# Performance work log

Measured on AMD Instinct MI355X. Metric: run time of the kernel, lower is better.

Reference implementation:

```python
import jax, jax.numpy as jnp
import numpy as np

B, L, D, H = 1, 2048, 1024, 16
DH = D // H            # head dim = 64
RD = 16                # rope dim = dim_head / 4 (partial RoPE)
SCALE = DH ** -0.5
NEG = -1e9


def _layernorm(x, g, b, eps=1e-5):
    m = jnp.mean(x, -1, keepdims=True)
    v = jnp.mean((x - m) ** 2, -1, keepdims=True)
    return (x - m) * jax.lax.rsqrt(v + eps) * g + b


def _rope_tables(length, rd):
    # GPT-NeoX style: freqs over rd/2, duplicated via concat
    inv_freq = 1.0 / (10000.0 ** (jnp.arange(0, rd, 2, dtype=jnp.float32) / rd))
    t = jnp.arange(length, dtype=jnp.float32)
    f = t[:, None] * inv_freq[None, :]          # [L, rd/2]
    f = jnp.concatenate([f, f], -1)             # [L, rd]
    return jnp.cos(f)[None, None], jnp.sin(f)[None, None]  # [1,1,L,rd]


def _apply_rope(x, cos, sin):
    # rotate only the first RD dims of each head; pass the rest through
    rd = cos.shape[-1]
    xr, xp = x[..., :rd], x[..., rd:]
    x1, x2 = jnp.split(xr, 2, axis=-1)
    rot = jnp.concatenate([-x2, x1], -1)
    return jnp.concatenate([xr * cos + rot * sin, xp], -1)


def _alibi_causal_bias(length, num_heads):
    # per-head ALiBi slope + causal mask (AttentionBiasMask: ['alibi','causal'])
    slopes = 2.0 ** (-8.0 * (jnp.arange(num_heads, dtype=jnp.float32) + 1) / num_heads)
    i = jnp.arange(length)
    rel = i[:, None] - i[None, :]               # [L, L], >=0 on/below diagonal
    bias = -slopes[:, None, None] * rel[None].astype(jnp.float32)
    bias = jnp.where(rel[None] >= 0, bias, NEG)  # causal mask
    return bias[None]                            # [1, H, L, L]


def setup_inputs() -> dict:
    key = jax.random.key(0)
    ks = jax.random.split(key, 8)
    s = 0.02
    return {
        "x": jax.random.normal(ks[0], (B, L, D), jnp.float32),
        "previous_attn_dots": jax.random.normal(ks[1], (B, H, L, L), jnp.float32) * 0.1,
        "Wq": jax.random.normal(ks[2], (D, D), jnp.float32) * s,
        "Wk": jax.random.normal(ks[3], (D, D), jnp.float32) * s,
        "Wv": jax.random.normal(ks[4], (D, D), jnp.float32) * s,
        "Wo": jax.random.normal(ks[5], (D, D), jnp.float32) * s,
        "bo": jnp.zeros((D,), jnp.float32),
        "gamma": jnp.ones((D,), jnp.float32),
        "beta": jnp.zeros((D,), jnp.float32),
        "Wg": jax.random.normal(ks[6], (D, D), jnp.float32) * s,
        "bg": jnp.zeros((D,), jnp.float32),
    }


def reference(x, previous_attn_dots, Wq, Wk, Wv, Wo, bo, gamma, beta, Wg, bg):
    residual = x
    cos, sin = _rope_tables(L, RD)
    bias = _alibi_causal_bias(L, H)

    h = _layernorm(x, gamma, beta)

    def heads(t):  # [B,L,D] -> [B,H,L,DH]
        return t.reshape(B, L, H, DH).transpose(0, 2, 1, 3)

    q = _apply_rope(heads(h @ Wq), cos, sin)
    k = _apply_rope(heads(h @ Wk), cos, sin)
    v = _apply_rope(heads(h @ Wv), cos, sin)  # rotate_v_bool=True

    dots = jnp.einsum('bhid,bhjd->bhij', q, k) * SCALE
    dots = dots + previous_attn_dots          # residual attention
    dots = dots + bias                        # ALiBi + causal
    attn_map = jax.nn.softmax(dots, axis=-1)

    o = jnp.einsum('bhij,bhjd->bhid', attn_map, v)
    o = o.transpose(0, 2, 1, 3).reshape(B, L, D)
    y = o @ Wo + bo

    gate = jax.nn.sigmoid(residual @ Wg + bg)  # output_gate ('sigmoid','on_residual')
    y = gate * y
    y = y + residual                           # add_residual
    return (y, attn_map, dots)
```

## Files before the change

### kernel.cpp

```cpp
#include <hip/hip_runtime.h>
#include <hip/hip_bf16.h>
#include <math.h>

#define LLEN 2048
#define DMODEL 1024
#define NHEAD 16
#define DHEAD 64
#define SCALE 0.125f
#define NEGF -1000000000.0f

typedef __attribute__((ext_vector_type(8))) short short8;
typedef __attribute__((ext_vector_type(4))) float f32x4;

__device__ __forceinline__ unsigned short f2bf(float f) {
  union { float f; unsigned u; } cv; cv.f = f;
  unsigned u = cv.u;
  u += 0x7FFF + ((u >> 16) & 1);
  return (unsigned short)(u >> 16);
}

__global__ __launch_bounds__(256) void transpose_w(
    const float* __restrict__ Wq, const float* __restrict__ Wk,
    const float* __restrict__ Wv, const float* __restrict__ Wo,
    const float* __restrict__ Wg,
    unsigned short* __restrict__ Wqt, unsigned short* __restrict__ Wkt,
    unsigned short* __restrict__ Wvt, unsigned short* __restrict__ Wot,
    unsigned short* __restrict__ Wgt) {
  const float* W; unsigned short* Wt;
  switch (blockIdx.z) {
    case 0: W = Wq; Wt = Wqt; break;
    case 1: W = Wk; Wt = Wkt; break;
    case 2: W = Wv; Wt = Wvt; break;
    case 3: W = Wo; Wt = Wot; break;
    default: W = Wg; Wt = Wgt; break;
  }
  __shared__ unsigned short tile[64][72];
  int k0 = blockIdx.y * 64, n0 = blockIdx.x * 64;
  int c4 = (threadIdx.x & 15) * 4, r = threadIdx.x >> 4;
  for (int rr = r; rr < 64; rr += 16) {
    float4 v = *(const float4*)(W + (size_t)(k0 + rr) * DMODEL + n0 + c4);
    tile[rr][c4 + 0] = f2bf(v.x); tile[rr][c4 + 1] = f2bf(v.y);
    tile[rr][c4 + 2] = f2bf(v.z); tile[rr][c4 + 3] = f2bf(v.w);
  }
  __syncthreads();
  for (int rr = r; rr < 64; rr += 16) {
    ushort4 o;
    o.x = tile[c4 + 0][rr]; o.y = tile[c4 + 1][rr];
    o.z = tile[c4 + 2][rr]; o.w = tile[c4 + 3][rr];
    *(ushort4*)(Wt + (size_t)(n0 + rr) * DMODEL + k0 + c4) = o;
  }
}

__global__ __launch_bounds__(256) void ln_kernel(
    const float* __restrict__ x, const float* __restrict__ gamma,
    const float* __restrict__ beta,
    unsigned short* __restrict__ hb, unsigned short* __restrict__ xb) {
  int l = blockIdx.x, t = threadIdx.x;
  float4 v = ((const float4*)(x + (size_t)l * DMODEL))[t];
  float s  = v.x + v.y + v.z + v.w;
  float s2 = v.x * v.x + v.y * v.y + v.z * v.z + v.w * v.w;
  for (int off = 32; off; off >>= 1) {
    s  += __shfl_down(s, off);
    s2 += __shfl_down(s2, off);
  }
  __shared__ float rs[4], rs2[4];
  int wave = t >> 6, lane = t & 63;
  if (lane == 0) { rs[wave] = s; rs2[wave] = s2; }
  __syncthreads();
  float mean = (rs[0] + rs[1] + rs[2] + rs[3]) * (1.0f / DMODEL);
  float var  = (rs2[0] + rs2[1] + rs2[2] + rs2[3]) * (1.0f / DMODEL) - mean * mean;
  float rstd = rsqrtf(var + 1e-5f);
  float4 g = ((const float4*)gamma)[t];
  float4 b = ((const float4*)beta)[t];
  ushort4 hh, xx;
  hh.x = f2bf((v.x - mean) * rstd * g.x + b.x);
  hh.y = f2bf((v.y - mean) * rstd * g.y + b.y);
  hh.z = f2bf((v.z - mean) * rstd * g.z + b.z);
  hh.w = f2bf((v.w - mean) * rstd * g.w + b.w);
  xx.x = f2bf(v.x); xx.y = f2bf(v.y); xx.z = f2bf(v.z); xx.w = f2bf(v.w);
  ((ushort4*)(hb + (size_t)l * DMODEL))[t] = hh;
  ((ushort4*)(xb + (size_t)l * DMODEL))[t] = xx;
}

__device__ __forceinline__ void mfma_gemm_64x64(
    const unsigned short* __restrict__ A, const unsigned short* __restrict__ Bt,
    int row0, int ncol0, int lm, int quad, f32x4 acc[4]) {
  for (int k0 = 0; k0 < DMODEL; k0 += 64) {
    short8 a0 = *(const short8*)(A + (size_t)(row0 + lm) * DMODEL + k0 + quad * 8);
    short8 a1 = *(const short8*)(A + (size_t)(row0 + lm) * DMODEL + k0 + 32 + quad * 8);
#pragma unroll
    for (int c = 0; c < 4; c++) {
      const unsigned short* bp = Bt + (size_t)(ncol0 + c * 16 + lm) * DMODEL + k0 + quad * 8;
      short8 b0 = *(const short8*)(bp);
      short8 b1 = *(const short8*)(bp + 32);
      acc[c] = __builtin_amdgcn_mfma_f32_16x16x32_bf16(a0, b0, acc[c], 0, 0, 0);
      acc[c] = __builtin_amdgcn_mfma_f32_16x16x32_bf16(a1, b1, acc[c], 0, 0, 0);
    }
  }
}

__global__ __launch_bounds__(256) void gemm_qkv(
    const unsigned short* __restrict__ hb,
    const unsigned short* __restrict__ Wqt, const unsigned short* __restrict__ Wkt,
    const unsigned short* __restrict__ Wvt,
    unsigned short* __restrict__ qb, unsigned short* __restrict__ kb,
    unsigned short* __restrict__ vT) {
  int which = blockIdx.z;
  const unsigned short* Bt = (which == 0) ? Wqt : (which == 1) ? Wkt : Wvt;
  int wave = threadIdx.x >> 6, lane = threadIdx.x & 63;
  int lm = lane & 15, quad = lane >> 4;
  int it = blockIdx.x, head = blockIdx.y;
  int row0 = it * 64 + wave * 16;
  f32x4 acc[4] = {};
  mfma_gemm_64x64(hb, Bt, row0, head * 64, lm, quad, acc);
  __shared__ float tile[64][65];
#pragma unroll
  for (int c = 0; c < 4; c++)
#pragma unroll
    for (int r2 = 0; r2 < 4; r2++)
      tile[wave * 16 + quad * 4 + r2][c * 16 + lm] = acc[c][r2];
  __syncthreads();
  int r = threadIdx.x >> 2, seg = threadIdx.x & 3;
  int lrow = it * 64 + r;
  float vals[16];
#pragma unroll
  for (int i2 = 0; i2 < 16; i2++) vals[i2] = tile[r][seg * 16 + i2];
  if (seg == 0) {
    float outv[16];
#pragma unroll
    for (int j = 0; j < 8; j++) {
      float invf = powf(10000.f, -(float)j * 0.125f);
      float f = (float)lrow * invf;
      float cs = cosf(f), sn = sinf(f);
      outv[j]     = vals[j] * cs - vals[j + 8] * sn;
      outv[j + 8] = vals[j + 8] * cs + vals[j] * sn;
    }
#pragma unroll
    for (int j = 0; j < 16; j++) vals[j] = outv[j];
  }
  if (which < 2) {
    unsigned short* dst = ((which == 0) ? qb : kb) + ((size_t)head * LLEN + lrow) * DHEAD + seg * 16;
    union { unsigned short u[16]; uint4 v[2]; } tmp;
#pragma unroll
    for (int i2 = 0; i2 < 16; i2++) tmp.u[i2] = f2bf(vals[i2]);
    *(uint4*)dst = tmp.v[0];
    *((uint4*)dst + 1) = tmp.v[1];
  } else {
    __syncthreads();
#pragma unroll
    for (int i2 = 0; i2 < 16; i2++) tile[r][seg * 16 + i2] = vals[i2];
    __syncthreads();
    int dh = threadIdx.x >> 2, ls = threadIdx.x & 3;
    union { unsigned short u[16]; uint4 v[2]; } tmp;
#pragma unroll
    for (int i2 = 0; i2 < 16; i2++) tmp.u[i2] = f2bf(tile[ls * 16 + i2][dh]);
    unsigned short* dst = vT + ((size_t)head * DHEAD + dh) * LLEN + it * 64 + ls * 16;
    *(uint4*)dst = tmp.v[0];
    *((uint4*)dst + 1) = tmp.v[1];
  }
}

__global__ __launch_bounds__(128) void attn_kernel(
    const unsigned short* __restrict__ qb, const unsigned short* __restrict__ kb,
    const unsigned short* __restrict__ vT, const float* __restrict__ prev,
    float* __restrict__ dots, unsigned short* __restrict__ ob,
    float* __restrict__ rinvg) {
  int h = blockIdx.y;
  int wv = threadIdx.x >> 6, lane = threadIdx.x & 63;
  int lm = lane & 15, quad = lane >> 4;
  int g0 = blockIdx.x * 2 + wv;
  const unsigned short* q = qb + (size_t)h * LLEN * DHEAD;
  const unsigned short* k = kb + (size_t)h * LLEN * DHEAD;
  const unsigned short* v = vT + (size_t)h * DHEAD * LLEN;
  const float* pr = prev + (size_t)h * LLEN * LLEN;
  float* drow = dots + (size_t)h * LLEN * LLEN;
  float slope = exp2f(-8.0f * (float)(h + 1) / (float)NHEAD);
  __shared__ __align__(16) unsigned short pt[2][16][72];

  for (int pass = 0; pass < 2; ++pass) {
    int g = pass ? (127 - g0) : g0;
    int row0 = g * 16;
    int jt_end = g >> 2;
    short8 qa0 = *(const short8*)(q + (size_t)(row0 + lm) * DHEAD + quad * 8);
    short8 qa1 = *(const short8*)(q + (size_t)(row0 + lm) * DHEAD + 32 + quad * 8);
    f32x4 oacc[4] = {};
    float lsum[4] = {0.f, 0.f, 0.f, 0.f};
    for (int jt = 0; jt <= jt_end; jt++) {
      f32x4 s[4];
#pragma unroll
      for (int c = 0; c < 4; c++) {
        const unsigned short* kp = k + (size_t)(jt * 64 + c * 16 + lm) * DHEAD + quad * 8;
        short8 b0 = *(const short8*)kp;
        short8 b1 = *(const short8*)(kp + 32);
        f32x4 z = {};
        z = __builtin_amdgcn_mfma_f32_16x16x32_bf16(qa0, b0, z, 0, 0, 0);
        z = __builtin_amdgcn_mfma_f32_16x16x32_bf16(qa1, b1, z, 0, 0, 0);
        s[c] = z;
      }
#pragma unroll
      for (int c = 0; c < 4; c++) {
        int j = jt * 64 + c * 16 + lm;
#pragma unroll
        for (int r = 0; r < 4; r++) {
          int i = row0 + quad * 4 + r;
          int rel = i - j;
          float bias = (rel >= 0) ? (-slope * (float)rel) : NEGF;
          float d = fmaf(s[c][r], SCALE, pr[(size_t)i * LLEN + j]) + bias;
          drow[(size_t)i * LLEN + j] = d;
          float p = __expf(d);
          lsum[r] += p;
          pt[wv][quad * 4 + r][c * 16 + lm] = f2bf(p);
        }
      }
      short8 pa0 = *(const short8*)&pt[wv][lm][quad * 8];
      short8 pa1 = *(const short8*)&pt[wv][lm][32 + quad * 8];
#pragma unroll
      for (int c = 0; c < 4; c++) {
        const unsigned short* vp = v + (size_t)(c * 16 + lm) * LLEN + jt * 64 + quad * 8;
        short8 b0 = *(const short8*)vp;
        short8 b1 = *(const short8*)(vp + 32);
        oacc[c] = __builtin_amdgcn_mfma_f32_16x16x32_bf16(pa0, b0, oacc[c], 0, 0, 0);
        oacc[c] = __builtin_amdgcn_mfma_f32_16x16x32_bf16(pa1, b1, oacc[c], 0, 0, 0);
      }
    }
    float rv[4];
#pragma unroll
    for (int r = 0; r < 4; r++) {
      float sm = lsum[r];
#pragma unroll
      for (int off = 1; off < 16; off <<= 1) sm += __shfl_xor(sm, off, 16);
      rv[r] = 1.0f / sm;
    }
#pragma unroll
    for (int c = 0; c < 4; c++)
#pragma unroll
      for (int r = 0; r < 4; r++)
        ob[(size_t)(row0 + quad * 4 + r) * DMODEL + h * DHEAD + c * 16 + lm] =
            f2bf(oacc[c][r] * rv[r]);
    if (lm == 0) {
#pragma unroll
      for (int r = 0; r < 4; r++)
        rinvg[(size_t)h * LLEN + row0 + quad * 4 + r] = rv[r];
    }
    int jstart = (jt_end + 1) * 64;
    int ncols4 = (LLEN - jstart) >> 2;
    if (ncols4 > 0) {
      float4 negv = {NEGF, NEGF, NEGF, NEGF};
      int r = lane >> 2, t4 = lane & 3;
      size_t base = (size_t)(row0 + r) * LLEN + jstart;
      for (int c4 = t4; c4 < ncols4; c4 += 4)
        *(float4*)(drow + base + c4 * 4) = negv;
    }
  }
}

__global__ __launch_bounds__(256) void attn_norm(
    const float* __restrict__ dots, const float* __restrict__ rinvg,
    float* __restrict__ attn) {
  int h = blockIdx.y;
  int i0 = blockIdx.x * 8;
  const float* dr = dots + (size_t)h * LLEN * LLEN;
  float* ar = attn + (size_t)h * LLEN * LLEN;
#pragma unroll
  for (int rr = 0; rr < 8; rr++) {
    int i = i0 + rr;
    float rinv = rinvg[(size_t)h * LLEN + i];
    int nwr4 = ((i >> 6) + 1) * 16;
#pragma unroll
    for (int jc = 0; jc < 2; jc++) {
      int j4 = threadIdx.x + jc * 256;
      size_t idx = (size_t)i * LLEN + (size_t)j4 * 4;
      if (j4 < nwr4) {
        float4 d = *(const float4*)(dr + idx);
        float4 o;
        o.x = __expf(d.x) * rinv;
        o.y = __expf(d.y) * rinv;
        o.z = __expf(d.z) * rinv;
        o.w = __expf(d.w) * rinv;
        *(float4*)(ar + idx) = o;
      } else {
        float4 z = {0.f, 0.f, 0.f, 0.f};
        *(float4*)(ar + idx) = z;
      }
    }
  }
}

__global__ __launch_bounds__(256) void gemm_gate(
    const unsigned short* __restrict__ xb, const unsigned short* __restrict__ Wgt,
    const float* __restrict__ bg, float* __restrict__ gate) {
  int wave = threadIdx.x >> 6, lane = threadIdx.x & 63;
  int lm = lane & 15, quad = lane >> 4;
  int row0 = blockIdx.x * 64 + wave * 16, ncol0 = blockIdx.y * 64;
  f32x4 acc[4] = {};
  mfma_gemm_64x64(xb, Wgt, row0, ncol0, lm, quad, acc);
#pragma unroll
  for (int c = 0; c < 4; c++) {
    int col = ncol0 + c * 16 + lm;
    float bgv = bg[col];
#pragma unroll
    for (int r = 0; r < 4; r++) {
      int i = row0 + quad * 4 + r;
      float g = acc[c][r] + bgv;
      gate[(size_t)i * DMODEL + col] = 1.0f / (1.0f + __expf(-g));
    }
  }
}

__global__ __launch_bounds__(256) void gemm_out(
    const unsigned short* __restrict__ ob, const unsigned short* __restrict__ Wot,
    const float* __restrict__ bo, const float* __restrict__ gate,
    const float* __restrict__ x, float* __restrict__ y) {
  int wave = threadIdx.x >> 6, lane = threadIdx.x & 63;
  int lm = lane & 15, quad = lane >> 4;
  int row0 = blockIdx.x * 64 + wave * 16, ncol0 = blockIdx.y * 64;
  f32x4 acc[4] = {};
  mfma_gemm_64x64(ob, Wot, row0, ncol0, lm, quad, acc);
#pragma unroll
  for (int c = 0; c < 4; c++) {
    int col = ncol0 + c * 16 + lm;
    float bov = bo[col];
#pragma unroll
    for (int r = 0; r < 4; r++) {
      int i = row0 + quad * 4 + r;
      size_t idx = (size_t)i * DMODEL + col;
      float y0 = acc[c][r] + bov;
      y[idx] = gate[idx] * y0 + x[idx];
    }
  }
}

extern "C" void kernel_launch(void* const* d_in, const int* in_sizes, int n_in,
                              void* d_out, int out_size, void* d_ws, size_t ws_size,
                              hipStream_t stream) {
  const float* x     = (const float*)d_in[0];
  const float* prev  = (const float*)d_in[1];
  const float* Wq    = (const float*)d_in[2];
  const float* Wk    = (const float*)d_in[3];
  const float* Wv    = (const float*)d_in[4];
  const float* Wo    = (const float*)d_in[5];
  const float* bo    = (const float*)d_in[6];
  const float* gamma = (const float*)d_in[7];
  const float* beta  = (const float*)d_in[8];
  const float* Wg    = (const float*)d_in[9];
  const float* bg    = (const float*)d_in[10];

  float* y    = (float*)d_out;
  float* attn = y + 2097152;
  float* dots = attn + 67108864;

  char* ws = (char*)d_ws;
  unsigned short* hb  = (unsigned short*)(ws + 0);
  unsigned short* xb  = (unsigned short*)(ws + 4194304);
  unsigned short* Wqt = (unsigned short*)(ws + 8388608);
  unsigned short* Wkt = (unsigned short*)(ws + 10485760);
  unsigned short* Wvt = (unsigned short*)(ws + 12582912);
  unsigned short* Wot = (unsigned short*)(ws + 14680064);
  unsigned short* Wgt = (unsigned short*)(ws + 16777216);
  unsigned short* qb  = (unsigned short*)(ws + 18874368);
  unsigned short* kb  = (unsigned short*)(ws + 23068672);
  unsigned short* vT  = (unsigned short*)(ws + 27262976);
  unsigned short* ob  = (unsigned short*)(ws + 31457280);
  float*          gate = (float*)(ws + 35651584);
  float*          rinvg = (float*)(ws + 0);

  transpose_w<<<dim3(16, 16, 5), 256, 0, stream>>>(Wq, Wk, Wv, Wo, Wg, Wqt, Wkt, Wvt, Wot, Wgt);
  ln_kernel<<<dim3(2048), 256, 0, stream>>>(x, gamma, beta, hb, xb);
  gemm_qkv<<<dim3(32, 16, 3), 256, 0, stream>>>(hb, Wqt, Wkt, Wvt, qb, kb, vT);
  attn_kernel<<<dim3(32, 16), 128, 0, stream>>>(qb, kb, vT, prev, dots, ob, rinvg);
  attn_norm<<<dim3(256, 16), 256, 0, stream>>>(dots, rinvg, attn);
  gemm_gate<<<dim3(32, 16), 256, 0, stream>>>(xb, Wgt, bg, gate);
  gemm_out<<<dim3(32, 16), 256, 0, stream>>>(ob, Wot, bo, gate, x, y);
}
```

Baseline: 1.216 ms.

## Split attention KV tiles across four waves per row block and fuse gate/out GEMMs

The attention kernel now gives each 16-row query block (per head) its own 256-thread block. The four waves stride over KV tiles and combine partial outputs and row sums through shared memory, replacing the earlier two-wave blocks that each paired two row groups for load balance. This exposes far more parallelism (2048 blocks) for the memory-bound dots/prev traffic, at the cost of an LDS reduction and reduced per-wave work. Separately, the gate GEMM and output GEMM are fused into one kernel, which removes the intermediate gate buffer write and read and one launch.

```diff
diff --git a/kernel.cpp b/kernel.cpp
--- a/kernel.cpp
+++ b/kernel.cpp
@@ -160,97 +160,114 @@
   }
 }
 
-__global__ __launch_bounds__(128) void attn_kernel(
+__global__ __launch_bounds__(256, 4) void attn_kernel(
     const unsigned short* __restrict__ qb, const unsigned short* __restrict__ kb,
     const unsigned short* __restrict__ vT, const float* __restrict__ prev,
     float* __restrict__ dots, unsigned short* __restrict__ ob,
     float* __restrict__ rinvg) {
-  int h = blockIdx.y;
+  int bid = blockIdx.x;
+  int h = bid & 15, g = bid >> 4;
   int wv = threadIdx.x >> 6, lane = threadIdx.x & 63;
   int lm = lane & 15, quad = lane >> 4;
-  int g0 = blockIdx.x * 2 + wv;
+  int row0 = g * 16;
+  int jt_end = g >> 2;
   const unsigned short* q = qb + (size_t)h * LLEN * DHEAD;
   const unsigned short* k = kb + (size_t)h * LLEN * DHEAD;
   const unsigned short* v = vT + (size_t)h * DHEAD * LLEN;
   const float* pr = prev + (size_t)h * LLEN * LLEN;
   float* drow = dots + (size_t)h * LLEN * LLEN;
   float slope = exp2f(-8.0f * (float)(h + 1) / (float)NHEAD);
-  __shared__ __align__(16) unsigned short pt[2][16][72];
-
-  for (int pass = 0; pass < 2; ++pass) {
-    int g = pass ? (127 - g0) : g0;
-    int row0 = g * 16;
-    int jt_end = g >> 2;
-    short8 qa0 = *(const short8*)(q + (size_t)(row0 + lm) * DHEAD + quad * 8);
-    short8 qa1 = *(const short8*)(q + (size_t)(row0 + lm) * DHEAD + 32 + quad * 8);
-    f32x4 oacc[4] = {};
-    float lsum[4] = {0.f, 0.f, 0.f, 0.f};
-    for (int jt = 0; jt <= jt_end; jt++) {
-      f32x4 s[4];
-#pragma unroll
-      for (int c = 0; c < 4; c++) {
-        const unsigned short* kp = k + (size_t)(jt * 64 + c * 16 + lm) * DHEAD + quad * 8;
-        short8 b0 = *(const short8*)kp;
-        short8 b1 = *(const short8*)(kp + 32);
-        f32x4 z = {};
-        z = __builtin_amdgcn_mfma_f32_16x16x32_bf16(qa0, b0, z, 0, 0, 0);
-        z = __builtin_amdgcn_mfma_f32_16x16x32_bf16(qa1, b1, z, 0, 0, 0);
-        s[c] = z;
+
+  __shared__ __align__(16) char smem[16640];
+  unsigned short (*pt)[16][72] = (unsigned short (*)[16][72])smem;
+  float (*red)[64][16] = (float (*)[64][16])smem;
+  float* redl = (float*)(smem + 16384);
+
+  short8 qa0 = *(const short8*)(q + (size_t)(row0 + lm) * DHEAD + quad * 8);
+  short8 qa1 = *(const short8*)(q + (size_t)(row0 + lm) * DHEAD + 32 + quad * 8);
+  f32x4 oacc[4] = {};
+  float lsum[4] = {0.f, 0.f, 0.f, 0.f};
+
+  for (int jt = wv; jt <= jt_end; jt += 4) {
+    f32x4 s[4];
+#pragma unroll
+    for (int c = 0; c < 4; c++) {
+      const unsigned short* kp = k + (size_t)(jt * 64 + c * 16 + lm) * DHEAD + quad * 8;
+      short8 b0 = *(const short8*)kp;
+      short8 b1 = *(const short8*)(kp + 32);
+      f32x4 z = {};
+      z = __builtin_amdgcn_mfma_f32_16x16x32_bf16(qa0, b0, z, 0, 0, 0);
+      z = __builtin_amdgcn_mfma_f32_16x16x32_bf16(qa1, b1, z, 0, 0, 0);
+      s[c] = z;
+    }
+#pragma unroll
+    for (int c = 0; c < 4; c++) {
+      int j = jt * 64 + c * 16 + lm;
+#pragma unroll
+      for (int r = 0; r < 4; r++) {
+        int i = row0 + quad * 4 + r;
+        int rel = i - j;
+        float bias = (rel >= 0) ? (-slope * (float)rel) : NEGF;
+        float d = fmaf(s[c][r], SCALE, pr[(size_t)i * LLEN + j]) + bias;
+        drow[(size_t)i * LLEN + j] = d;
+        float p = __expf(d);
+        lsum[r] += p;
+        pt[wv][quad * 4 + r][c * 16 + lm] = f2bf(p);
       }
-#pragma unroll
-      for (int c = 0; c < 4; c++) {
-        int j = jt * 64 + c * 16 + lm;
-#pragma unroll
-        for (int r = 0; r < 4; r++) {
-          int i = row0 + quad * 4 + r;
-          int rel = i - j;
-          float bias = (rel >= 0) ? (-slope * (float)rel) : NEGF;
-          float d = fmaf(s[c][r], SCALE, pr[(size_t)i * LLEN + j]) + bias;
-          drow[(size_t)i * LLEN + j] = d;
-          float p = __expf(d);
-          lsum[r] += p;
-          pt[wv][quad * 4 + r][c * 16 + lm] = f2bf(p);
-        }
-      }
-      short8 pa0 = *(const short8*)&pt[wv][lm][quad * 8];
-      short8 pa1 = *(const short8*)&pt[wv][lm][32 + quad * 8];
-#pragma unroll
-      for (int c = 0; c < 4; c++) {
-        const unsigned short* vp = v + (size_t)(c * 16 + lm) * LLEN + jt * 64 + quad * 8;
-        short8 b0 = *(const short8*)vp;
-        short8 b1 = *(const short8*)(vp + 32);
-        oacc[c] = __builtin_amdgcn_mfma_f32_16x16x32_bf16(pa0, b0, oacc[c], 0, 0, 0);
-        oacc[c] = __builtin_amdgcn_mfma_f32_16x16x32_bf16(pa1, b1, oacc[c], 0, 0, 0);
-      }
-    }
-    float rv[4];
-#pragma unroll
-    for (int r = 0; r < 4; r++) {
-      float sm = lsum[r];
-#pragma unroll
-      for (int off = 1; off < 16; off <<= 1) sm += __shfl_xor(sm, off, 16);
-      rv[r] = 1.0f / sm;
-    }
-#pragma unroll
-    for (int c = 0; c < 4; c++)
-#pragma unroll
-      for (int r = 0; r < 4; r++)
-        ob[(size_t)(row0 + quad * 4 + r) * DMODEL + h * DHEAD + c * 16 + lm] =
-            f2bf(oacc[c][r] * rv[r]);
-    if (lm == 0) {
-#pragma unroll
-      for (int r = 0; r < 4; r++)
-        rinvg[(size_t)h * LLEN + row0 + quad * 4 + r] = rv[r];
-    }
-    int jstart = (jt_end + 1) * 64;
-    int ncols4 = (LLEN - jstart) >> 2;
-    if (ncols4 > 0) {
-      float4 negv = {NEGF, NEGF, NEGF, NEGF};
-      int r = lane >> 2, t4 = lane & 3;
-      size_t base = (size_t)(row0 + r) * LLEN + jstart;
-      for (int c4 = t4; c4 < ncols4; c4 += 4)
-        *(float4*)(drow + base + c4 * 4) = negv;
-    }
+    }
+    short8 pa0 = *(const short8*)&pt[wv][lm][quad * 8];
+    short8 pa1 = *(const short8*)&pt[wv][lm][32 + quad * 8];
+#pragma unroll
+    for (int c = 0; c < 4; c++) {
+      const unsigned short* vp = v + (size_t)(c * 16 + lm) * LLEN + jt * 64 + quad * 8;
+      short8 b0 = *(const short8*)vp;
+      short8 b1 = *(const short8*)(vp + 32);
+      oacc[c] = __builtin_amdgcn_mfma_f32_16x16x32_bf16(pa0, b0, oacc[c], 0, 0, 0);
+      oacc[c] = __builtin_amdgcn_mfma_f32_16x16x32_bf16(pa1, b1, oacc[c], 0, 0, 0);
+    }
+  }
+#pragma unroll
+  for (int r = 0; r < 4; r++) {
+#pragma unroll
+    for (int off = 1; off < 16; off <<= 1) lsum[r] += __shfl_xor(lsum[r], off, 16);
+  }
+  __syncthreads();
+#pragma unroll
+  for (int c = 0; c < 4; c++)
+#pragma unroll
+    for (int r = 0; r < 4; r++)
+      red[wv][lane][c * 4 + r] = oacc[c][r];
+  if (lm == 0) {
+#pragma unroll
+    for (int r = 0; r < 4; r++) redl[wv * 16 + quad * 4 + r] = lsum[r];
+  }
+  __syncthreads();
+  {
+    int t = threadIdx.x;
+    int ln = t & 63, idx0 = t >> 6;
+    int qd = ln >> 4, lmm = ln & 15;
+#pragma unroll
+    for (int kk = 0; kk < 4; kk++) {
+      int idx = idx0 * 4 + kk;
+      int c = idx >> 2, r = idx & 3;
+      float sv = red[0][ln][idx] + red[1][ln][idx] + red[2][ln][idx] + red[3][ln][idx];
+      int rr = qd * 4 + r;
+      float rs = redl[rr] + redl[16 + rr] + redl[32 + rr] + redl[48 + rr];
+      ob[(size_t)(row0 + rr) * DMODEL + h * DHEAD + c * 16 + lmm] = f2bf(sv / rs);
+    }
+    if (t < 16) {
+      float rs = redl[t] + redl[16 + t] + redl[32 + t] + redl[48 + t];
+      rinvg[(size_t)h * LLEN + row0 + t] = 1.0f / rs;
+    }
+  }
+  int jstart = (jt_end + 1) * 64;
+  int ncols4 = (LLEN - jstart) >> 2;
+  if (ncols4 > 0) {
+    float4 negv = {NEGF, NEGF, NEGF, NEGF};
+    int r = threadIdx.x >> 4, t16 = threadIdx.x & 15;
+    size_t base = (size_t)(row0 + r) * LLEN + jstart;
+    for (int c4 = t16; c4 < ncols4; c4 += 16)
+      *(float4*)(drow + base + c4 * 4) = negv;
   }
 }
 
@@ -286,46 +303,45 @@
   }
 }
 
-__global__ __launch_bounds__(256) void gemm_gate(
+__global__ __launch_bounds__(256) void gemm_gateout(
     const unsigned short* __restrict__ xb, const unsigned short* __restrict__ Wgt,
-    const float* __restrict__ bg, float* __restrict__ gate) {
-  int wave = threadIdx.x >> 6, lane = threadIdx.x & 63;
-  int lm = lane & 15, quad = lane >> 4;
-  int row0 = blockIdx.x * 64 + wave * 16, ncol0 = blockIdx.y * 64;
-  f32x4 acc[4] = {};
-  mfma_gemm_64x64(xb, Wgt, row0, ncol0, lm, quad, acc);
-#pragma unroll
-  for (int c = 0; c < 4; c++) {
-    int col = ncol0 + c * 16 + lm;
-    float bgv = bg[col];
-#pragma unroll
-    for (int r = 0; r < 4; r++) {
-      int i = row0 + quad * 4 + r;
-      float g = acc[c][r] + bgv;
-      gate[(size_t)i * DMODEL + col] = 1.0f / (1.0f + __expf(-g));
-    }
-  }
-}
-
-__global__ __launch_bounds__(256) void gemm_out(
+    const float* __restrict__ bg,
     const unsigned short* __restrict__ ob, const unsigned short* __restrict__ Wot,
-    const float* __restrict__ bo, const float* __restrict__ gate,
+    const float* __restrict__ bo,
     const float* __restrict__ x, float* __restrict__ y) {
   int wave = threadIdx.x >> 6, lane = threadIdx.x & 63;
   int lm = lane & 15, quad = lane >> 4;
   int row0 = blockIdx.x * 64 + wave * 16, ncol0 = blockIdx.y * 64;
-  f32x4 acc[4] = {};
-  mfma_gemm_64x64(ob, Wot, row0, ncol0, lm, quad, acc);
+  f32x4 accg[4] = {}, acco[4] = {};
+  for (int k0 = 0; k0 < DMODEL; k0 += 64) {
+    short8 ax0 = *(const short8*)(xb + (size_t)(row0 + lm) * DMODEL + k0 + quad * 8);
+    short8 ax1 = *(const short8*)(xb + (size_t)(row0 + lm) * DMODEL + k0 + 32 + quad * 8);
+    short8 ao0 = *(const short8*)(ob + (size_t)(row0 + lm) * DMODEL + k0 + quad * 8);
+    short8 ao1 = *(const short8*)(ob + (size_t)(row0 + lm) * DMODEL + k0 + 32 + quad * 8);
+#pragma unroll
+    for (int c = 0; c < 4; c++) {
+      const unsigned short* bgp = Wgt + (size_t)(ncol0 + c * 16 + lm) * DMODEL + k0 + quad * 8;
+      const unsigned short* bop = Wot + (size_t)(ncol0 + c * 16 + lm) * DMODEL + k0 + quad * 8;
+      short8 g0 = *(const short8*)(bgp);
+      short8 g1 = *(const short8*)(bgp + 32);
+      short8 o0 = *(const short8*)(bop);
+      short8 o1 = *(const short8*)(bop + 32);
+      accg[c] = __builtin_amdgcn_mfma_f32_16x16x32_bf16(ax0, g0, accg[c], 0, 0, 0);
+      acco[c] = __builtin_amdgcn_mfma_f32_16x16x32_bf16(ao0, o0, acco[c], 0, 0, 0);
+      accg[c] = __builtin_amdgcn_mfma_f32_16x16x32_bf16(ax1, g1, accg[c], 0, 0, 0);
+      acco[c] = __builtin_amdgcn_mfma_f32_16x16x32_bf16(ao1, o1, acco[c], 0, 0, 0);
+    }
+  }
 #pragma unroll
   for (int c = 0; c < 4; c++) {
     int col = ncol0 + c * 16 + lm;
-    float bov = bo[col];
+    float bgv = bg[col], bov = bo[col];
 #pragma unroll
     for (int r = 0; r < 4; r++) {
       int i = row0 + quad * 4 + r;
       size_t idx = (size_t)i * DMODEL + col;
-      float y0 = acc[c][r] + bov;
-      y[idx] = gate[idx] * y0 + x[idx];
+      float gt = 1.0f / (1.0f + __expf(-(accg[c][r] + bgv)));
+      y[idx] = gt * (acco[c][r] + bov) + x[idx];
     }
   }
 }
@@ -361,14 +377,12 @@
   unsigned short* kb  = (unsigned short*)(ws + 23068672);
   unsigned short* vT  = (unsigned short*)(ws + 27262976);
   unsigned short* ob  = (unsigned short*)(ws + 31457280);
-  float*          gate = (float*)(ws + 35651584);
   float*          rinvg = (float*)(ws + 0);
 
   transpose_w<<<dim3(16, 16, 5), 256, 0, stream>>>(Wq, Wk, Wv, Wo, Wg, Wqt, Wkt, Wvt, Wot, Wgt);
   ln_kernel<<<dim3(2048), 256, 0, stream>>>(x, gamma, beta, hb, xb);
   gemm_qkv<<<dim3(32, 16, 3), 256, 0, stream>>>(hb, Wqt, Wkt, Wvt, qb, kb, vT);
-  attn_kernel<<<dim3(32, 16), 128, 0, stream>>>(qb, kb, vT, prev, dots, ob, rinvg);
+  attn_kernel<<<dim3(2048), 256, 0, stream>>>(qb, kb, vT, prev, dots, ob, rinvg);
   attn_norm<<<dim3(256, 16), 256, 0, stream>>>(dots, rinvg, attn);
-  gemm_gate<<<dim3(32, 16), 256, 0, stream>>>(xb, Wgt, bg, gate);
-  gemm_out<<<dim3(32, 16), 256, 0, stream>>>(ob, Wot, bo, gate, x, y);
-}
+  gemm_gateout<<<dim3(32, 16), 256, 0, stream>>>(xb, Wgt, bg, ob, Wot, bo, x, y);
+}
```

Measured after the change: 1.030 ms. 15.3% less time.
